# Kernel optimization log

Measured on AMD Instinct MI355X. Metric: run time of the kernel, lower is better.

Reference implementation:

```python
import jax, jax.numpy as jnp
import numpy as np
from jax import lax

# ---- helpers ----

def conv2d(x, w, b, p):
    # x: NCHW, w: OIHW
    y = lax.conv_general_dilated(x, w, (1, 1), [(p, p), (p, p)],
                                 dimension_numbers=('NCHW', 'OIHW', 'NCHW'))
    return y + b.reshape(1, -1, 1, 1)


def bn_eval(x, g, be, m, v):
    # BatchNorm2d in inference mode, eps=1e-5 (torch default)
    inv = lax.rsqrt(v + 1e-5)
    return (x - m.reshape(1, -1, 1, 1)) * (g * inv).reshape(1, -1, 1, 1) + be.reshape(1, -1, 1, 1)


def gelu(x):
    return jax.nn.gelu(x, approximate=False)  # torch nn.GELU default is exact


def up2(x):
    # bilinear upsample x2 with align_corners=True (nn.UpsamplingBilinear2d)
    B, C, H, W = x.shape
    def coords(n):
        N = 2 * n
        s = jnp.arange(N, dtype=jnp.float32) * (float(n - 1) / float(N - 1))
        i0 = jnp.floor(s).astype(jnp.int32)
        i1 = jnp.minimum(i0 + 1, n - 1)
        wgt = (s - i0.astype(jnp.float32)).astype(x.dtype)
        return i0, i1, wgt
    y0, y1, wy = coords(H)
    x0, x1, wx = coords(W)
    r = x[:, :, y0, :] * (1.0 - wy)[:, None] + x[:, :, y1, :] * wy[:, None]
    r = r[:, :, :, x0] * (1.0 - wx) + r[:, :, :, x1] * wx
    return r


def avg_pool2(x):
    return lax.reduce_window(x, 0.0, lax.add, (1, 1, 2, 2), (1, 1, 2, 2), 'VALID') * 0.25


def max_pool2(x):
    return lax.reduce_window(x, -jnp.inf, lax.max, (1, 1, 2, 2), (1, 1, 2, 2), 'VALID')


def dilate3(x):
    # cv2.dilate with ones(3,3), 1 iteration == 3x3 max filter, stride 1, SAME
    return lax.reduce_window(x, -jnp.inf, lax.max, (1, 1, 3, 3), (1, 1, 1, 1), 'SAME')


def ap_mp(x1, x2):
    # AP_MP: L2 norm over channels of (avgpool(x1) - maxpool(x2)) -> [B,1,h,w]
    d = avg_pool2(x1) - max_pool2(x2)
    return jnp.sqrt(jnp.sum(d * d, axis=1, keepdims=True))


def setup_inputs() -> dict:
    key = jax.random.key(0)
    ks = jax.random.split(key, 40)
    B, C1, C2, H, W = 8, 64, 128, 192, 192
    h, w = H // 2, W // 2
    f = jnp.float32

    def conv_w(k, o, i, kh):
        return jax.random.normal(k, (o, i, kh, kh), f) * (1.0 / np.sqrt(i * kh * kh))

    def bn_p(k, c):
        k1, k2, k3, k4 = jax.random.split(k, 4)
        return (jax.random.uniform(k1, (c,), f, 0.5, 1.5),
                jax.random.normal(k2, (c,), f) * 0.1,
                jax.random.normal(k3, (c,), f) * 0.1,
                jax.random.uniform(k4, (c,), f, 0.5, 1.5))

    g_up, be_up, m_up, v_up = bn_p(ks[10], C1)
    g_d1, be_d1, m_d1, v_d1 = bn_p(ks[11], C1)
    g_d2, be_d2, m_d2, v_d2 = bn_p(ks[12], C1)
    g_d3, be_d3, m_d3, v_d3 = bn_p(ks[13], C1)

    return {
        'x': jax.random.normal(ks[0], (B, C1, H, W), f),
        'small_x': jax.random.normal(ks[1], (B, C2, h, w), f),
        'in_map': jax.random.normal(ks[2], (B, 1, h, w), f),
        'W_up': conv_w(ks[3], C1, C2, 7), 'b_up': jax.random.normal(ks[4], (C1,), f) * 0.01,
        'g_up': g_up, 'be_up': be_up, 'm_up': m_up, 'v_up': v_up,
        'W_c2': conv_w(ks[5], C1, C1, 3), 'b_c2': jax.random.normal(ks[6], (C1,), f) * 0.01,
        'W_d1': conv_w(ks[7], C1, 2 * C1, 3), 'b_d1': jax.random.normal(ks[8], (C1,), f) * 0.01,
        'g_d1': g_d1, 'be_d1': be_d1, 'm_d1': m_d1, 'v_d1': v_d1,
        'W_d2': conv_w(ks[14], C1, C1, 3), 'b_d2': jax.random.normal(ks[15], (C1,), f) * 0.01,
        'g_d2': g_d2, 'be_d2': be_d2, 'm_d2': m_d2, 'v_d2': v_d2,
        'W_d3': conv_w(ks[16], C1, C1, 3), 'b_d3': jax.random.normal(ks[17], (C1,), f) * 0.01,
        'g_d3': g_d3, 'be_d3': be_d3, 'm_d3': m_d3, 'v_d3': v_d3,
        'W_out': conv_w(ks[18], 1, C1, 7), 'b_out': jax.random.normal(ks[19], (1,), f) * 0.01,
        'beta': jnp.ones((1,), f),
    }


def reference(x, small_x, in_map,
              W_up, b_up, g_up, be_up, m_up, v_up,
              W_c2, b_c2,
              W_d1, b_d1, g_d1, be_d1, m_d1, v_d1,
              W_d2, b_d2, g_d2, be_d2, m_d2, v_d2,
              W_d3, b_d3, g_d3, be_d3, m_d3, v_d3,
              W_out, b_out, beta):
    # self.up: conv7x7 C2->C1, BN, GELU, bilinear up x2
    small = up2(gelu(bn_eval(conv2d(small_x, W_up, b_up, 3), g_up, be_up, m_up, v_up)))

    # AP_MP based uncertainty map (conv_context_* outputs are unused in forward)
    diff_map = ap_mp(small, x) + ap_mp(x, small)         # [B,1,H/2,W/2]

    input_map = jax.nn.sigmoid(up2(in_map))              # [B,1,H,W]
    diff_map = jax.nn.sigmoid(up2(diff_map))             # [B,1,H,W]

    # focus_background=True path: morphological dilation (3x3, 1 iter) minus map
    increase_map = dilate3(input_map) - input_map
    difference_map = dilate3(diff_map) - diff_map
    b_feature = x * (increase_map + difference_map + 1.0)

    fn = conv2d(b_feature, W_c2, b_c2, 1)
    r = jnp.concatenate([small, beta.reshape(()) * fn], axis=1)
    r = gelu(bn_eval(conv2d(r, W_d1, b_d1, 1), g_d1, be_d1, m_d1, v_d1))
    r = gelu(bn_eval(conv2d(r, W_d2, b_d2, 1), g_d2, be_d2, m_d2, v_d2))
    r = gelu(bn_eval(conv2d(r, W_d3, b_d3, 1), g_d3, be_d3, m_d3, v_d3))
    output_map = conv2d(r, W_out, b_out, 3)
    return (r, output_map)
```

## Files before the change

kernel.cpp:

```cpp
#include <hip/hip_runtime.h>
#include <math.h>


#define DI __device__ __forceinline__

typedef __attribute__((ext_vector_type(8))) short short8;
typedef __attribute__((ext_vector_type(4))) float floatx4;

DI float gelu_f(float x) {
  float u = x * (1.5957691216f + 0.0713548162f * x * x);
  return x / (1.0f + __expf(-u));
}

DI unsigned short f2b(float f) {
  unsigned u = __float_as_uint(f);
  u += 0x7FFFu + ((u >> 16) & 1u);
  return (unsigned short)(u >> 16);
}
DI unsigned pack2(float a, float b) {
  return (unsigned)f2b(a) | ((unsigned)f2b(b) << 16);
}
DI float b2f(short s) { return __uint_as_float(((unsigned)(unsigned short)s) << 16); }

__global__ void epi_prep_k(const float* __restrict__ bias,
                           const float* __restrict__ g, const float* __restrict__ be,
                           const float* __restrict__ m, const float* __restrict__ v,
                           const float* __restrict__ betap, int useBN,
                           float* __restrict__ A, float* __restrict__ B) {
  int oc = threadIdx.x;
  if (oc >= 64) return;
  if (useBN) {
    float giv = g[oc] * rsqrtf(v[oc] + 1e-5f);
    A[oc] = giv;
    B[oc] = (bias[oc] - m[oc]) * giv + be[oc];
  } else {
    float bt = betap[0];
    A[oc] = bt;
    B[oc] = bias[oc] * bt;
  }
}

__global__ void frag3_k(const float* __restrict__ W, short* __restrict__ wf,
                        int CIN, int icg0) {
  int i = blockIdx.x * 256 + threadIdx.x;
  if (i >= 18 * 4 * 64 * 8) return;
  int j = i & 7; int lane = (i >> 3) & 63; int nt = (i >> 9) & 3; int s = i >> 11;
  int q = lane >> 4, r16 = lane & 15;
  int tap = s >> 1, ich = s & 1;
  int ky = tap / 3, kx = tap % 3;
  int ic = icg0 + ich * 32 + q * 8 + j;
  int oc = (r16 >> 2) * 16 + nt * 4 + (r16 & 3);
  wf[i] = (short)f2b(W[((oc * CIN + ic) * 3 + ky) * 3 + kx]);
}

__global__ void frag_up_k(const float* __restrict__ W, short* __restrict__ wf) {
  int i = blockIdx.x * 256 + threadIdx.x;
  if (i >= 196 * 4 * 64 * 8) return;
  int j = i & 7; int lane = (i >> 3) & 63; int nt = (i >> 9) & 3; int s = i >> 11;
  int q = lane >> 4, r16 = lane & 15;
  int pass = s / 49, tap = s % 49;
  int ky = tap / 7, kx = tap % 7;
  int ic = pass * 32 + q * 8 + j;
  int oc = nt * 16 + r16;
  wf[i] = (short)f2b(W[((oc * 128 + ic) * 7 + ky) * 7 + kx]);
}

__global__ void frag_out_k(const float* __restrict__ W, short* __restrict__ wf) {
  int i = blockIdx.x * 256 + threadIdx.x;
  if (i >= 98 * 64 * 8) return;
  int j = i & 7; int lane = (i >> 3) & 63; int s = i >> 9;
  int q = lane >> 4;
  int ich = s / 49, tap = s - ich * 49;
  int ch = ich * 32 + q * 8 + j;
  int ky = tap / 7, kx = tap - ky * 7;
  wf[i] = (short)f2b(W[ch * 49 + ky * 7 + kx]);
}

__global__ void to_nhwc_k(const float* __restrict__ in, short* __restrict__ out,
                          int C8, int HW, int total) {
  int i = blockIdx.x * 256 + threadIdx.x;
  if (i >= total) return;
  int cu = i % C8; int p = i / C8;
  int b = p / HW; int pix = p % HW;
  const float* src = in + ((size_t)b * C8 * 8 + cu * 8) * HW + pix;
  int4 o;
  unsigned* op = (unsigned*)&o;
  #pragma unroll
  for (int j = 0; j < 4; ++j)
    op[j] = pack2(src[(2 * j) * (size_t)HW], src[(2 * j + 1) * (size_t)HW]);
  *reinterpret_cast<int4*>(out + (size_t)p * C8 * 8 + cu * 8) = o;
}

template <bool TWO_IN, bool SCALE_IN, bool GELU_OUT, bool OUT_NCHW, bool OUT_BOTH>
__global__ __launch_bounds__(256, 3) void conv3h_k(
    const short* __restrict__ inA, const short* __restrict__ inB,
    const short* __restrict__ wfrag,
    const float* __restrict__ Aepi, const float* __restrict__ Bepi,
    const float* __restrict__ scale,
    short* __restrict__ outH, float* __restrict__ outF)
{
  const int H = 192;
  int bi = blockIdx.x;
  int tx = bi % 6, t2 = bi / 6, ty = t2 % 24, b = t2 / 24;
  int x0 = tx * 32, y0 = ty * 8;
  int tid = threadIdx.x;
  int w = tid >> 6, lane = tid & 63, q = lane >> 4, r16 = lane & 15;

  __shared__ __align__(16) short s_in[340 * 72];
  const short8* wf = (const short8*)wfrag;

  floatx4 acc[4][4];
  #pragma unroll
  for (int a = 0; a < 4; ++a)
    #pragma unroll
    for (int c = 0; c < 4; ++c) acc[a][c] = (floatx4){0.f, 0.f, 0.f, 0.f};

  for (int half = 0; half < (TWO_IN ? 2 : 1); ++half) {
    const short* src = half ? inB : inA;
    if (half) __syncthreads();
    for (int u = tid; u < 2720; u += 256) {
      int px = u >> 3, cu = u & 7;
      int yy = px / 34, xx = px - yy * 34;
      int gy = y0 + yy - 1, gx = x0 + xx - 1;
      int4 v = make_int4(0, 0, 0, 0);
      if (gy >= 0 && gy < H && gx >= 0 && gx < H) {
        v = *reinterpret_cast<const int4*>(src + (((size_t)b * H + gy) * H + gx) * 64 + cu * 8);
        if (SCALE_IN) {
          float sc = scale[((size_t)b * H + gy) * H + gx];
          short* sp = (short*)&v;
          #pragma unroll
          for (int j = 0; j < 8; ++j) sp[j] = (short)f2b(b2f(sp[j]) * sc);
        }
      }
      *reinterpret_cast<int4*>(&s_in[px * 72 + cu * 8]) = v;
    }
    __syncthreads();

    const short8* wfh = wf + half * (18 * 4 * 64);
    short8 wcur[4];
    #pragma unroll
    for (int ot = 0; ot < 4; ++ot) wcur[ot] = wfh[ot * 64 + lane];
    #pragma unroll
    for (int s = 0; s < 18; ++s) {
      short8 wnxt[4];
      if (s < 17) {
        #pragma unroll
        for (int ot = 0; ot < 4; ++ot) wnxt[ot] = wfh[((s + 1) * 4 + ot) * 64 + lane];
      }
      int tap = s >> 1, ich = s & 1;
      int ky = tap / 3, kx = tap - ky * 3;
      #pragma unroll
      for (int yt = 0; yt < 2; ++yt) {
        #pragma unroll
        for (int xh = 0; xh < 2; ++xh) {
          int iy = w * 2 + yt + ky;
          int ix = xh * 16 + r16 + kx;
          short8 pfr = *reinterpret_cast<const short8*>(
              &s_in[(iy * 34 + ix) * 72 + ich * 32 + q * 8]);
          #pragma unroll
          for (int ot = 0; ot < 4; ++ot)
            acc[yt * 2 + xh][ot] =
                __builtin_amdgcn_mfma_f32_16x16x32_bf16(wcur[ot], pfr, acc[yt * 2 + xh][ot], 0, 0, 0);
        }
      }
      #pragma unroll
      for (int ot = 0; ot < 4; ++ot) wcur[ot] = wnxt[ot];
    }
  }

  float4 Af[4], Bf[4];
  #pragma unroll
  for (int ot = 0; ot < 4; ++ot) {
    Af[ot] = *reinterpret_cast<const float4*>(Aepi + q * 16 + ot * 4);
    Bf[ot] = *reinterpret_cast<const float4*>(Bepi + q * 16 + ot * 4);
  }
  #pragma unroll
  for (int yt = 0; yt < 2; ++yt) {
    int gy = y0 + w * 2 + yt;
    float va[2][16];
    #pragma unroll
    for (int xh = 0; xh < 2; ++xh) {
      #pragma unroll
      for (int ot = 0; ot < 4; ++ot) {
        const int g = yt * 2 + xh;
        float v0 = acc[g][ot][0] * Af[ot].x + Bf[ot].x;
        float v1 = acc[g][ot][1] * Af[ot].y + Bf[ot].y;
        float v2 = acc[g][ot][2] * Af[ot].z + Bf[ot].z;
        float v3 = acc[g][ot][3] * Af[ot].w + Bf[ot].w;
        if (GELU_OUT) { v0 = gelu_f(v0); v1 = gelu_f(v1); v2 = gelu_f(v2); v3 = gelu_f(v3); }
        va[xh][ot * 4 + 0] = v0;
        va[xh][ot * 4 + 1] = v1;
        va[xh][ot * 4 + 2] = v2;
        va[xh][ot * 4 + 3] = v3;
      }
    }
    if (OUT_NCHW) {
      #pragma unroll
      for (int idx = 0; idx < 16; ++idx) {
        int oc = q * 16 + idx;
        size_t base = (((size_t)b * 64 + oc) * H + gy) * H + x0 + r16;
        outF[base] = va[0][idx];
        outF[base + 16] = va[1][idx];
      }
    }
    if (!OUT_NCHW || OUT_BOTH) {
      #pragma unroll
      for (int xh = 0; xh < 2; ++xh) {
        int4 o0, o1;
        unsigned* p0 = (unsigned*)&o0;
        unsigned* p1 = (unsigned*)&o1;
        #pragma unroll
        for (int j = 0; j < 4; ++j) {
          p0[j] = pack2(va[xh][2 * j], va[xh][2 * j + 1]);
          p1[j] = pack2(va[xh][8 + 2 * j], va[xh][8 + 2 * j + 1]);
        }
        short* dst = outH + (((size_t)b * H + gy) * H + x0 + xh * 16 + r16) * 64 + q * 16;
        *reinterpret_cast<int4*>(dst) = o0;
        *reinterpret_cast<int4*>(dst + 8) = o1;
      }
    }
  }
}

__global__ __launch_bounds__(256, 4) void conv_up_h_k(
    const short* __restrict__ in,
    const short* __restrict__ wfrag,
    float* __restrict__ part)
{
  const int H = 96;
  int bi = blockIdx.x;
  int pass = bi & 3; int tile = bi >> 2;
  int tx = tile % 6, t2 = tile / 6, ty = t2 % 6, b = t2 / 6;
  int x0 = tx * 16, y0 = ty * 16;
  int tid = threadIdx.x;
  int w = tid >> 6, lane = tid & 63, q = lane >> 4, r16 = lane & 15;

  __shared__ __align__(16) short s_in[484 * 40];
  const short8* wf = (const short8*)wfrag;

  floatx4 acc[4][4];
  #pragma unroll
  for (int a = 0; a < 4; ++a)
    #pragma unroll
    for (int c = 0; c < 4; ++c) acc[a][c] = (floatx4){0.f, 0.f, 0.f, 0.f};

  for (int u = tid; u < 1936; u += 256) {
    int px = u >> 2, cu = u & 3;
    int yy = px / 22, xx = px - yy * 22;
    int gy = y0 + yy - 3, gx = x0 + xx - 3;
    int4 v = make_int4(0, 0, 0, 0);
    if (gy >= 0 && gy < H && gx >= 0 && gx < H)
      v = *reinterpret_cast<const int4*>(
          in + (((size_t)b * H + gy) * H + gx) * 128 + pass * 32 + cu * 8);
    *reinterpret_cast<int4*>(&s_in[px * 40 + cu * 8]) = v;
  }
  __syncthreads();

  const short8* wfp = wf + pass * (49 * 4 * 64);
  short8 wcur[4];
  #pragma unroll
  for (int ot = 0; ot < 4; ++ot) wcur[ot] = wfp[ot * 64 + lane];
  for (int s = 0; s < 49; ++s) {
    short8 wnxt[4];
    if (s < 48) {
      #pragma unroll
      for (int ot = 0; ot < 4; ++ot) wnxt[ot] = wfp[((s + 1) * 4 + ot) * 64 + lane];
    }
    int ky = s / 7, kx = s - ky * 7;
    #pragma unroll
    for (int yt = 0; yt < 4; ++yt) {
      int iy = w * 4 + yt + ky;
      int ix = r16 + kx;
      short8 pfr = *reinterpret_cast<const short8*>(&s_in[(iy * 22 + ix) * 40 + q * 8]);
      #pragma unroll
      for (int ot = 0; ot < 4; ++ot)
        acc[yt][ot] = __builtin_amdgcn_mfma_f32_16x16x32_bf16(wcur[ot], pfr, acc[yt][ot], 0, 0, 0);
    }
    #pragma unroll
    for (int ot = 0; ot < 4; ++ot) wcur[ot] = wnxt[ot];
  }

  float* dst = part + (size_t)pass * 4718592;
  #pragma unroll
  for (int yt = 0; yt < 4; ++yt) {
    int gy = y0 + w * 4 + yt;
    #pragma unroll
    for (int ot = 0; ot < 4; ++ot) {
      float4 o;
      o.x = acc[yt][ot][0]; o.y = acc[yt][ot][1];
      o.z = acc[yt][ot][2]; o.w = acc[yt][ot][3];
      *reinterpret_cast<float4*>(
          &dst[(((size_t)b * H + gy) * H + x0 + r16) * 64 + ot * 16 + q * 4]) = o;
    }
  }
}

__global__ void reduce_up_k(const float* __restrict__ part,
                            const float* __restrict__ A, const float* __restrict__ B,
                            short* __restrict__ out)
{
  int i8 = blockIdx.x * 256 + threadIdx.x;
  if (i8 >= 589824) return;
  size_t base = (size_t)i8 * 8;
  const size_t N = 4718592;
  float s[8];
  #pragma unroll
  for (int j = 0; j < 8; ++j) s[j] = 0.f;
  #pragma unroll
  for (int p = 0; p < 4; ++p) {
    float4 a = *reinterpret_cast<const float4*>(part + p * N + base);
    float4 bq = *reinterpret_cast<const float4*>(part + p * N + base + 4);
    s[0] += a.x; s[1] += a.y; s[2] += a.z; s[3] += a.w;
    s[4] += bq.x; s[5] += bq.y; s[6] += bq.z; s[7] += bq.w;
  }
  int oc0 = (int)(base & 63);
  int4 o;
  unsigned* op = (unsigned*)&o;
  #pragma unroll
  for (int j = 0; j < 4; ++j) {
    float va = gelu_f(s[2 * j] * A[oc0 + 2 * j] + B[oc0 + 2 * j]);
    float vb = gelu_f(s[2 * j + 1] * A[oc0 + 2 * j + 1] + B[oc0 + 2 * j + 1]);
    op[j] = pack2(va, vb);
  }
  *reinterpret_cast<int4*>(out + base) = o;
}

__global__ void up2h_k(const short* __restrict__ in, short* __restrict__ out) {
  int i = blockIdx.x * 256 + threadIdx.x;
  if (i >= 2359296) return;
  int cu = i & 7; int p = i >> 3;
  int x = p % 192; int t = p / 192; int y = t % 192; int b = t / 192;
  const float c95 = 95.0f / 191.0f;
  float sy = y * c95; int y0i = (int)sy; int y1i = min(y0i + 1, 95); float wy = sy - (float)y0i;
  float sx = x * c95; int x0i = (int)sx; int x1i = min(x0i + 1, 95); float wx = sx - (float)x0i;
  const short* base = in + (size_t)b * 96 * 96 * 64;
  int4 a00 = *reinterpret_cast<const int4*>(base + (y0i * 96 + x0i) * 64 + cu * 8);
  int4 a01 = *reinterpret_cast<const int4*>(base + (y0i * 96 + x1i) * 64 + cu * 8);
  int4 a10 = *reinterpret_cast<const int4*>(base + (y1i * 96 + x0i) * 64 + cu * 8);
  int4 a11 = *reinterpret_cast<const int4*>(base + (y1i * 96 + x1i) * 64 + cu * 8);
  const short* s00 = (const short*)&a00; const short* s01 = (const short*)&a01;
  const short* s10 = (const short*)&a10; const short* s11 = (const short*)&a11;
  float w00 = (1.f - wy) * (1.f - wx), w01 = (1.f - wy) * wx;
  float w10 = wy * (1.f - wx), w11 = wy * wx;
  int4 o;
  unsigned* op = (unsigned*)&o;
  #pragma unroll
  for (int j = 0; j < 4; ++j) {
    float va = b2f(s00[2 * j]) * w00 + b2f(s01[2 * j]) * w01 +
               b2f(s10[2 * j]) * w10 + b2f(s11[2 * j]) * w11;
    float vb = b2f(s00[2 * j + 1]) * w00 + b2f(s01[2 * j + 1]) * w01 +
               b2f(s10[2 * j + 1]) * w10 + b2f(s11[2 * j + 1]) * w11;
    op[j] = pack2(va, vb);
  }
  *reinterpret_cast<int4*>(out + (size_t)p * 64 + cu * 8) = o;
}

__global__ void pools_h_k(const short* __restrict__ small, const short* __restrict__ xh,
                          float* __restrict__ out) {
  int i = blockIdx.x * 256 + threadIdx.x;
  if (i >= 73728) return;
  int x96 = i % 96; int y96 = (i / 96) % 96; int b = i / 9216;
  size_t base = (((size_t)b * 192 + 2 * y96) * 192 + 2 * x96) * 64;
  const int RS = 192 * 64;
  float s1 = 0.f, s2 = 0.f;
  for (int cu = 0; cu < 8; ++cu) {
    int4 sa0 = *reinterpret_cast<const int4*>(small + base + cu * 8);
    int4 sa1 = *reinterpret_cast<const int4*>(small + base + 64 + cu * 8);
    int4 sa2 = *reinterpret_cast<const int4*>(small + base + RS + cu * 8);
    int4 sa3 = *reinterpret_cast<const int4*>(small + base + RS + 64 + cu * 8);
    int4 xa0 = *reinterpret_cast<const int4*>(xh + base + cu * 8);
    int4 xa1 = *reinterpret_cast<const int4*>(xh + base + 64 + cu * 8);
    int4 xa2 = *reinterpret_cast<const int4*>(xh + base + RS + cu * 8);
    int4 xa3 = *reinterpret_cast<const int4*>(xh + base + RS + 64 + cu * 8);
    const short* p0 = (const short*)&sa0; const short* p1 = (const short*)&sa1;
    const short* p2 = (const short*)&sa2; const short* p3 = (const short*)&sa3;
    const short* q0 = (const short*)&xa0; const short* q1 = (const short*)&xa1;
    const short* q2 = (const short*)&xa2; const short* q3 = (const short*)&xa3;
    #pragma unroll
    for (int j = 0; j < 8; ++j) {
      float a0 = b2f(p0[j]), a1 = b2f(p1[j]), a2 = b2f(p2[j]), a3 = b2f(p3[j]);
      float b0 = b2f(q0[j]), b1 = b2f(q1[j]), b2 = b2f(q2[j]), b3 = b2f(q3[j]);
      float avgS = 0.25f * (a0 + a1 + a2 + a3);
      float maxS = fmaxf(fmaxf(a0, a1), fmaxf(a2, a3));
      float avgX = 0.25f * (b0 + b1 + b2 + b3);
      float maxX = fmaxf(fmaxf(b0, b1), fmaxf(b2, b3));
      float d1 = avgS - maxX; s1 = fmaf(d1, d1, s1);
      float d2 = avgX - maxS; s2 = fmaf(d2, d2, s2);
    }
  }
  out[((size_t)b * 96 + y96) * 96 + x96] = sqrtf(s1) + sqrtf(s2);
}

template <bool SIG>
__global__ void up2_k(const float* __restrict__ in, float* __restrict__ out, int total) {
  int i = blockIdx.x * 256 + threadIdx.x;
  if (i >= total) return;
  int x = i % 192; int y = (i / 192) % 192; int bc = i / (192 * 192);
  const float c95 = 95.0f / 191.0f;
  float sy = y * c95; int y0 = (int)sy; int y1 = min(y0 + 1, 95); float wy = sy - (float)y0;
  float sx = x * c95; int x0 = (int)sx; int x1 = min(x0 + 1, 95); float wx = sx - (float)x0;
  const float* p = in + (size_t)bc * 96 * 96;
  float v00 = p[y0 * 96 + x0], v01 = p[y0 * 96 + x1];
  float v10 = p[y1 * 96 + x0], v11 = p[y1 * 96 + x1];
  float v = (1.0f - wx) * ((1.0f - wy) * v00 + wy * v10) +
            wx * ((1.0f - wy) * v01 + wy * v11);
  if (SIG) v = 1.0f / (1.0f + expf(-v));
  out[i] = v;
}

__global__ void scale_k(const float* __restrict__ iM, const float* __restrict__ dM,
                        float* __restrict__ out) {
  int i = blockIdx.x * 256 + threadIdx.x;
  if (i >= 8 * 192 * 192) return;
  int x = i % 192; int y = (i / 192) % 192; int b = i / (192 * 192);
  const float* pi = iM + (size_t)b * 192 * 192;
  const float* pd = dM + (size_t)b * 192 * 192;
  float mi = -1e30f, md = -1e30f;
  for (int dy = -1; dy <= 1; ++dy) {
    int yy = y + dy;
    if (yy < 0 || yy >= 192) continue;
    for (int dx = -1; dx <= 1; ++dx) {
      int xx = x + dx;
      if (xx < 0 || xx >= 192) continue;
      mi = fmaxf(mi, pi[yy * 192 + xx]);
      md = fmaxf(md, pd[yy * 192 + xx]);
    }
  }
  out[i] = (mi - pi[y * 192 + x]) + (md - pd[y * 192 + x]) + 1.0f;
}

__global__ __launch_bounds__(256, 4) void conv_out_mfma_k(
    const short* __restrict__ in,
    const short* __restrict__ wfB,
    const float* __restrict__ bias,
    float* __restrict__ out)
{
  const int H = 192;
  int bi = blockIdx.x;
  int tx = bi % 12, t2 = bi / 12, ty = t2 % 12, b = t2 / 12;
  int x0 = tx * 16, y0 = ty * 16;
  int tid = threadIdx.x;
  int w = tid >> 6, lane = tid & 63, q = lane >> 4, r16 = lane & 15;

  __shared__ __align__(16) short s_in[484 * 36];
  const short8* wf = (const short8*)wfB;

  floatx4 acc[4];
  #pragma unroll
  for (int yt = 0; yt < 4; ++yt) acc[yt] = (floatx4){0.f, 0.f, 0.f, 0.f};

  for (int ich = 0; ich < 2; ++ich) {
    if (ich) __syncthreads();
    for (int u = tid; u < 1936; u += 256) {
      int px = u >> 2, cu = u & 3;
      int yy = px / 22, xx = px - yy * 22;
      int gy = y0 + yy - 3, gx = x0 + xx - 3;
      int4 v = make_int4(0, 0, 0, 0);
      if (gy >= 0 && gy < H && gx >= 0 && gx < H)
        v = *reinterpret_cast<const int4*>(
            in + (((size_t)b * H + gy) * H + gx) * 64 + ich * 32 + cu * 8);
      *reinterpret_cast<int4*>(&s_in[px * 36 + cu * 8]) = v;
    }
    __syncthreads();

    const short8* wfi = wf + ich * (49 * 64);
    short8 wcur = wfi[lane];
    for (int s = 0; s < 49; ++s) {
      short8 wnxt;
      if (s < 48) wnxt = wfi[(s + 1) * 64 + lane];
      int ky = s / 7, kx = s - ky * 7;
      #pragma unroll
      for (int yt = 0; yt < 4; ++yt) {
        int iy = w * 4 + yt + ky;
        int ix = r16 + kx;
        short8 pfr = *reinterpret_cast<const short8*>(
            &s_in[(iy * 22 + ix) * 36 + q * 8]);
        acc[yt] = __builtin_amdgcn_mfma_f32_16x16x32_bf16(pfr, wcur, acc[yt], 0, 0, 0);
      }
      wcur = wnxt;
    }
  }

  float b0 = bias[0];
  if (r16 == 0) {
    #pragma unroll
    for (int yt = 0; yt < 4; ++yt) {
      int gy = y0 + w * 4 + yt;
      float4 o = make_float4(acc[yt][0] + b0, acc[yt][1] + b0,
                             acc[yt][2] + b0, acc[yt][3] + b0);
      *reinterpret_cast<float4*>(&out[((size_t)b * H + gy) * H + x0 + q * 4]) = o;
    }
  }
}

extern "C" void kernel_launch(void* const* d_in, const int* in_sizes, int n_in,
                              void* d_out, int out_size, void* d_ws, size_t ws_size,
                              hipStream_t stream) {
  (void)in_sizes; (void)n_in; (void)out_size; (void)ws_size;
  const float* x       = (const float*)d_in[0];
  const float* small_x = (const float*)d_in[1];
  const float* in_map  = (const float*)d_in[2];
  const float* W_up = (const float*)d_in[3];  const float* b_up = (const float*)d_in[4];
  const float* g_up = (const float*)d_in[5];  const float* be_up = (const float*)d_in[6];
  const float* m_up = (const float*)d_in[7];  const float* v_up = (const float*)d_in[8];
  const float* W_c2 = (const float*)d_in[9];  const float* b_c2 = (const float*)d_in[10];
  const float* W_d1 = (const float*)d_in[11]; const float* b_d1 = (const float*)d_in[12];
  const float* g_d1 = (const float*)d_in[13]; const float* be_d1 = (const float*)d_in[14];
  const float* m_d1 = (const float*)d_in[15]; const float* v_d1 = (const float*)d_in[16];
  const float* W_d2 = (const float*)d_in[17]; const float* b_d2 = (const float*)d_in[18];
  const float* g_d2 = (const float*)d_in[19]; const float* be_d2 = (const float*)d_in[20];
  const float* m_d2 = (const float*)d_in[21]; const float* v_d2 = (const float*)d_in[22];
  const float* W_d3 = (const float*)d_in[23]; const float* b_d3 = (const float*)d_in[24];
  const float* g_d3 = (const float*)d_in[25]; const float* be_d3 = (const float*)d_in[26];
  const float* m_d3 = (const float*)d_in[27]; const float* v_d3 = (const float*)d_in[28];
  const float* W_out = (const float*)d_in[29]; const float* b_out = (const float*)d_in[30];
  const float* beta = (const float*)d_in[31];

  const size_t SZ = 18874368;
  float* ws = (float*)d_ws;
  float* partU = ws;
  short* fnh   = (short*)partU;
  short* rh3   = fnh;
  short* r2h   = fnh + 18874368;
  float* p1 = ws + 18874368;
  short* xh  = (short*)p1;
  float* p2 = p1 + 9437184;
  short* sxh = (short*)p2;
  float* p3 = p2 + 4718592;
  short* t0h = (short*)p3;
  short* wf_out = t0h;
  float* p4 = p3 + 2359296;
  short* smallh = (short*)p4;
  float* p5 = p4 + 9437184;
  short* r1h = (short*)p5;
  float* p6 = p5 + 9437184;
  float* diff96 = p6;
  float* iMap   = diff96 + 73728;
  float* dMap   = iMap + 294912;
  float* scaleM = dMap + 294912;
  float* pA = scaleM + 294912;
  float* A_up = pA;        float* B_up = pA + 64;
  float* A_c2 = pA + 128;  float* B_c2 = pA + 192;
  float* A_d1 = pA + 256;  float* B_d1 = pA + 320;
  float* A_d2 = pA + 384;  float* B_d2 = pA + 448;
  float* A_d3 = pA + 512;  float* B_d3 = pA + 576;
  short* wf_up = (short*)(pA + 640);
  short* wf_c2 = wf_up + 401408;
  short* wf_d1 = wf_c2 + 36864;
  short* wf_d2 = wf_d1 + 73728;
  short* wf_d3 = wf_d2 + 36864;

  float* out0 = (float*)d_out;
  float* out1 = out0 + SZ;

  epi_prep_k<<<1, 64, 0, stream>>>(b_up, g_up, be_up, m_up, v_up, nullptr, 1, A_up, B_up);
  epi_prep_k<<<1, 64, 0, stream>>>(b_c2, nullptr, nullptr, nullptr, nullptr, beta, 0, A_c2, B_c2);
  epi_prep_k<<<1, 64, 0, stream>>>(b_d1, g_d1, be_d1, m_d1, v_d1, nullptr, 1, A_d1, B_d1);
  epi_prep_k<<<1, 64, 0, stream>>>(b_d2, g_d2, be_d2, m_d2, v_d2, nullptr, 1, A_d2, B_d2);
  epi_prep_k<<<1, 64, 0, stream>>>(b_d3, g_d3, be_d3, m_d3, v_d3, nullptr, 1, A_d3, B_d3);
  frag_up_k<<<1568, 256, 0, stream>>>(W_up, wf_up);
  frag3_k<<<144, 256, 0, stream>>>(W_c2, wf_c2, 64, 0);
  frag3_k<<<144, 256, 0, stream>>>(W_d1, wf_d1, 128, 0);
  frag3_k<<<144, 256, 0, stream>>>(W_d1, wf_d1 + 36864, 128, 64);
  frag3_k<<<144, 256, 0, stream>>>(W_d2, wf_d2, 64, 0);
  frag3_k<<<144, 256, 0, stream>>>(W_d3, wf_d3, 64, 0);
  to_nhwc_k<<<9216, 256, 0, stream>>>(x, xh, 8, 36864, 2359296);
  to_nhwc_k<<<4608, 256, 0, stream>>>(small_x, sxh, 16, 9216, 1179648);

  conv_up_h_k<<<1152, 256, 0, stream>>>(sxh, wf_up, partU);
  reduce_up_k<<<2304, 256, 0, stream>>>(partU, A_up, B_up, t0h);
  up2h_k<<<9216, 256, 0, stream>>>(t0h, smallh);
  frag_out_k<<<196, 256, 0, stream>>>(W_out, wf_out);

  pools_h_k<<<288, 256, 0, stream>>>(smallh, xh, diff96);
  up2_k<true><<<1152, 256, 0, stream>>>(in_map, iMap, 8 * 192 * 192);
  up2_k<true><<<1152, 256, 0, stream>>>(diff96, dMap, 8 * 192 * 192);
  scale_k<<<1152, 256, 0, stream>>>(iMap, dMap, scaleM);

  conv3h_k<false, true, false, false, false><<<1152, 256, 0, stream>>>(
      xh, nullptr, wf_c2, A_c2, B_c2, scaleM, fnh, nullptr);
  conv3h_k<true, false, true, false, false><<<1152, 256, 0, stream>>>(
      smallh, fnh, wf_d1, A_d1, B_d1, nullptr, r1h, nullptr);
  conv3h_k<false, false, true, false, false><<<1152, 256, 0, stream>>>(
      r1h, nullptr, wf_d2, A_d2, B_d2, nullptr, r2h, nullptr);
  conv3h_k<false, false, true, true, true><<<1152, 256, 0, stream>>>(
      r2h, nullptr, wf_d3, A_d3, B_d3, nullptr, rh3, out0);

  conv_out_mfma_k<<<1152, 256, 0, stream>>>(rh3, wf_out, b_out, out1);
}
```

Before: 697.1 us.

## Store conv_up partial sums in bf16 and swizzle block order across XCDs

```diff
diff --git a/kernel.cpp b/kernel.cpp
--- a/kernel.cpp
+++ b/kernel.cpp
@@ -100,7 +100,7 @@
     short* __restrict__ outH, float* __restrict__ outF)
 {
   const int H = 192;
-  int bi = blockIdx.x;
+  int bi = (blockIdx.x & 7) * 144 + (blockIdx.x >> 3);
   int tx = bi % 6, t2 = bi / 6, ty = t2 % 24, b = t2 / 24;
   int x0 = tx * 32, y0 = ty * 8;
   int tid = threadIdx.x;
@@ -225,10 +225,10 @@
 __global__ __launch_bounds__(256, 4) void conv_up_h_k(
     const short* __restrict__ in,
     const short* __restrict__ wfrag,
-    float* __restrict__ part)
+    short* __restrict__ part)
 {
   const int H = 96;
-  int bi = blockIdx.x;
+  int bi = (blockIdx.x & 7) * 144 + (blockIdx.x >> 3);
   int pass = bi & 3; int tile = bi >> 2;
   int tx = tile % 6, t2 = tile / 6, ty = t2 % 6, b = t2 / 6;
   int x0 = tx * 16, y0 = ty * 16;
@@ -280,22 +280,22 @@
     for (int ot = 0; ot < 4; ++ot) wcur[ot] = wnxt[ot];
   }
 
-  float* dst = part + (size_t)pass * 4718592;
+  short* dst = part + (size_t)pass * 4718592;
   #pragma unroll
   for (int yt = 0; yt < 4; ++yt) {
     int gy = y0 + w * 4 + yt;
     #pragma unroll
     for (int ot = 0; ot < 4; ++ot) {
-      float4 o;
-      o.x = acc[yt][ot][0]; o.y = acc[yt][ot][1];
-      o.z = acc[yt][ot][2]; o.w = acc[yt][ot][3];
-      *reinterpret_cast<float4*>(
-          &dst[(((size_t)b * H + gy) * H + x0 + r16) * 64 + ot * 16 + q * 4]) = o;
-    }
-  }
-}
-
-__global__ void reduce_up_k(const float* __restrict__ part,
+      uint2 pk;
+      pk.x = pack2(acc[yt][ot][0], acc[yt][ot][1]);
+      pk.y = pack2(acc[yt][ot][2], acc[yt][ot][3]);
+      *reinterpret_cast<uint2*>(
+          &dst[(((size_t)b * H + gy) * H + x0 + r16) * 64 + ot * 16 + q * 4]) = pk;
+    }
+  }
+}
+
+__global__ void reduce_up_k(const short* __restrict__ part,
                             const float* __restrict__ A, const float* __restrict__ B,
                             short* __restrict__ out)
 {
@@ -308,10 +308,10 @@
   for (int j = 0; j < 8; ++j) s[j] = 0.f;
   #pragma unroll
   for (int p = 0; p < 4; ++p) {
-    float4 a = *reinterpret_cast<const float4*>(part + p * N + base);
-    float4 bq = *reinterpret_cast<const float4*>(part + p * N + base + 4);
-    s[0] += a.x; s[1] += a.y; s[2] += a.z; s[3] += a.w;
-    s[4] += bq.x; s[5] += bq.y; s[6] += bq.z; s[7] += bq.w;
+    int4 a = *reinterpret_cast<const int4*>(part + p * N + base);
+    const short* ap = (const short*)&a;
+    #pragma unroll
+    for (int j = 0; j < 8; ++j) s[j] += b2f(ap[j]);
   }
   int oc0 = (int)(base & 63);
   int4 o;
@@ -436,7 +436,7 @@
     float* __restrict__ out)
 {
   const int H = 192;
-  int bi = blockIdx.x;
+  int bi = (blockIdx.x & 7) * 144 + (blockIdx.x >> 3);
   int tx = bi % 12, t2 = bi / 12, ty = t2 % 12, b = t2 / 12;
   int x0 = tx * 16, y0 = ty * 16;
   int tid = threadIdx.x;
@@ -519,6 +519,7 @@
   const size_t SZ = 18874368;
   float* ws = (float*)d_ws;
   float* partU = ws;
+  short* partUh = (short*)partU;
   short* fnh   = (short*)partU;
   short* rh3   = fnh;
   short* r2h   = fnh + 18874368;
@@ -567,8 +568,8 @@
   to_nhwc_k<<<9216, 256, 0, stream>>>(x, xh, 8, 36864, 2359296);
   to_nhwc_k<<<4608, 256, 0, stream>>>(small_x, sxh, 16, 9216, 1179648);
 
-  conv_up_h_k<<<1152, 256, 0, stream>>>(sxh, wf_up, partU);
-  reduce_up_k<<<2304, 256, 0, stream>>>(partU, A_up, B_up, t0h);
+  conv_up_h_k<<<1152, 256, 0, stream>>>(sxh, wf_up, partUh);
+  reduce_up_k<<<2304, 256, 0, stream>>>(partUh, A_up, B_up, t0h);
   up2h_k<<<9216, 256, 0, stream>>>(t0h, smallh);
   frag_out_k<<<196, 256, 0, stream>>>(W_out, wf_out);
 
```

After: 665.8 us. 1.05x faster.
